# Performance work log

Measured on AMD Instinct MI355X. Metric: run time of the kernel, lower is better.

## Reference

```python
import jax, jax.numpy as jnp
import numpy as np

E = 8        # n_experts
TOP_K = 2    # n_activated_experts
B, T, C = 4, 2048, 2048   # batch, seq, d_model
F = 5632     # expert FFN hidden (SwiGLU)


def setup_inputs() -> dict:
    key = jax.random.key(0)
    k = jax.random.split(key, 5)
    s = 0.02  # init scale keeps activations sane
    return {
        "x":  jax.random.normal(k[0], (B, T, C), jnp.float32),
        "Wg": jax.random.normal(k[1], (C, E), jnp.float32) * s,   # gate Linear (no bias)
        "W1": jax.random.normal(k[2], (E, C, F), jnp.float32) * s, # expert gate proj
        "W3": jax.random.normal(k[3], (E, C, F), jnp.float32) * s, # expert up proj
        "W2": jax.random.normal(k[4], (E, F, C), jnp.float32) * s, # expert down proj
    }


def _moe(x, Wg, W1, W3, W2, top_k=TOP_K, norm_probs=True):
    Bb, Tt, Cc = x.shape
    xf = x.reshape(-1, Cc)                                   # [N, C]
    logits = xf @ Wg                                         # [N, E]
    probs = jax.nn.softmax(logits.astype(jnp.float32), axis=-1)
    probs, indices = jax.lax.top_k(probs, top_k)             # [N, K]
    if norm_probs:
        probs = probs / probs.sum(axis=-1, keepdims=True)
    probs = probs.astype(x.dtype)
    N, Ee = xf.shape[0], W1.shape[0]
    # per-token combine weights: w[n, e] = prob if expert e selected for token n else 0
    # (top_k indices are distinct per token, so at most one add per (n, e))
    w = jnp.zeros((N, Ee), x.dtype).at[jnp.arange(N)[:, None], indices].add(probs)
    # scan over experts: weight-0 tokens contribute nothing, matching the sparse
    # masked dispatch/scatter-add of the original exactly.
    def body(y, ws):
        w1, w3, w2, we = ws                                   # we: [N]
        h = jax.nn.silu(xf @ w1) * (xf @ w3)                  # [N, F]
        return y + we[:, None] * (h @ w2), None
    y, _ = jax.lax.scan(body, jnp.zeros_like(xf), (W1, W3, W2, w.T))
    return y.reshape(Bb, Tt, Cc)


def reference(x, Wg, W1, W3, W2):
    return _moe(x, Wg, W1, W3, W2)
```

## Files before the change

kernel.cpp:

```cpp
#include <hip/hip_runtime.h>

#define N_TOK 8192
#define C_DIM 2048
#define F_DIM 5632
#define E_NUM 8

#define BM 128
#define BN 128
#define BK 64
#define MAXT 136
#define GRID1 (MAXT * (F_DIM/BN))
#define GRID2 (MAXT * (C_DIM/BN))

typedef __attribute__((ext_vector_type(8))) short bf16x8;
typedef __attribute__((ext_vector_type(4))) float f32x4;

typedef const void __attribute__((address_space(1)))* gas1;
typedef void __attribute__((address_space(3)))* las3;

__device__ __forceinline__ unsigned short f2bf(float f){
  union { float f; unsigned u; } v; v.f = f;
  unsigned r = v.u + 0x7FFFu + ((v.u >> 16) & 1u);
  return (unsigned short)(r >> 16);
}

__device__ __forceinline__ void glds16(const unsigned short* g, unsigned short* l){
  __builtin_amdgcn_global_load_lds((gas1)g, (las3)l, 16, 0, 0);
}

__global__ void k_cvt_x(const float* __restrict__ x, unsigned short* __restrict__ xb, int n4){
  int i = blockIdx.x * blockDim.x + threadIdx.x;
  int stride = gridDim.x * blockDim.x;
  const float4* xi = (const float4*)x;
  ushort4* xo = (ushort4*)xb;
  for (; i < n4; i += stride){
    float4 v = xi[i];
    ushort4 o; o.x = f2bf(v.x); o.y = f2bf(v.y); o.z = f2bf(v.z); o.w = f2bf(v.w);
    xo[i] = o;
  }
}

__global__ void k_tcvt_w(const float* __restrict__ in, unsigned short* __restrict__ out, int R, int Cc){
  __shared__ float t[64][65];
  size_t slab = (size_t)blockIdx.z * R * Cc;
  in += slab; out += slab;
  int c0 = blockIdx.x * 64, r0 = blockIdx.y * 64;
  int tx = threadIdx.x, ty = threadIdx.y;
  #pragma unroll
  for (int i = 0; i < 16; ++i){
    int r = ty + i*4;
    t[r][tx] = in[(size_t)(r0 + r) * Cc + c0 + tx];
  }
  __syncthreads();
  #pragma unroll
  for (int i = 0; i < 16; ++i){
    int cr = ty + i*4;
    out[(size_t)(c0 + cr) * R + r0 + tx] = f2bf(t[tx][cr]);
  }
}

__global__ void k_router(const float* __restrict__ x, const float* __restrict__ Wg,
                         int* __restrict__ cnt, int* __restrict__ list, float* __restrict__ p_slot)
{
  int wid = threadIdx.x >> 6, lane = threadIdx.x & 63;
  int n = blockIdx.x * 4 + wid;
  int e = lane >> 3, sub = lane & 7;
  const float* xr = x + (size_t)n * C_DIM;
  float acc = 0.f;
  for (int i = sub; i < C_DIM; i += 8)
    acc += xr[i] * Wg[i*E_NUM + e];
  acc += __shfl_xor(acc, 1);
  acc += __shfl_xor(acc, 2);
  acc += __shfl_xor(acc, 4);
  float lg[E_NUM];
  #pragma unroll
  for (int j = 0; j < E_NUM; ++j) lg[j] = __shfl(acc, j*8);
  if (lane == 0){
    int e1 = 0; float m1 = lg[0];
    #pragma unroll
    for (int j = 1; j < E_NUM; ++j) if (lg[j] > m1){ m1 = lg[j]; e1 = j; }
    int e2 = -1; float m2 = -1e30f;
    #pragma unroll
    for (int j = 0; j < E_NUM; ++j) if (j != e1 && lg[j] > m2){ m2 = lg[j]; e2 = j; }
    float p1 = 1.f / (1.f + __expf(m2 - m1));
    float p2 = 1.f - p1;
    int pos1 = atomicAdd(&cnt[e1], 1);
    list[e1*N_TOK + pos1] = n*2;
    p_slot[n*2] = p1;
    int pos2 = atomicAdd(&cnt[e2], 1);
    list[e2*N_TOK + pos2] = n*2 + 1;
    p_slot[n*2 + 1] = p2;
  }
}

__global__ void k_prefix(const int* __restrict__ cnt, int* __restrict__ meta){
  if (threadIdx.x == 0 && blockIdx.x == 0){
    int acc = 0, t = 0;
    for (int e = 0; e < E_NUM; ++e){
      meta[e] = acc; acc += cnt[e];
      int nt = (cnt[e] + BM - 1) / BM;
      for (int i = 0; i < nt; ++i) meta[16 + t++] = (e << 16) | i;
    }
    meta[8] = t;
  }
}

__global__ __launch_bounds__(256, 2) void k_gemm1(
    const unsigned short* __restrict__ xb,
    const unsigned short* __restrict__ wb1,
    const unsigned short* __restrict__ wb3,
    unsigned short* __restrict__ h,
    const int* __restrict__ cnt,
    const int* __restrict__ meta,
    const int* __restrict__ list)
{
  int o = blockIdx.x;
  int w = (o & 7) * (GRID1/8) + (o >> 3);
  int t = w % MAXT;
  int n0 = (w / MAXT) * BN;
  if (t >= meta[8]) return;
  int info = meta[16 + t];
  int e  = info >> 16;
  int m0 = (info & 0xffff) * BM;
  int count = cnt[e];
  int hbase = meta[e];

  __shared__ __align__(16) unsigned short sA [BM*BK];
  __shared__ __align__(16) unsigned short sB1[BN*BK];
  __shared__ __align__(16) unsigned short sB3[BN*BK];

  int tid = threadIdx.x;
  int lane = tid & 63, wid = tid >> 6;
  int wm = wid >> 1, wn = wid & 1;

  const unsigned short* aS[4];
  const unsigned short* bS[4];
  int swz = (((tid & 7) ^ ((tid >> 3) & 7))) * 8;
  #pragma unroll
  for (int it = 0; it < 4; ++it){
    int row = it*32 + (tid >> 3);
    int ts  = list[e*N_TOK + m0 + row];
    int tok = (ts >> 1) & (N_TOK - 1);
    aS[it] = xb + (size_t)tok * C_DIM + swz;
    bS[it] = wb1 + ((size_t)e*F_DIM + n0 + row) * C_DIM + swz;
  }
  ptrdiff_t w31 = wb3 - wb1;

  f32x4 zero = {0.f, 0.f, 0.f, 0.f};
  f32x4 acc1[4][4], acc3[4][4];
  #pragma unroll
  for (int mi = 0; mi < 4; ++mi)
    #pragma unroll
    for (int ni = 0; ni < 4; ++ni){ acc1[mi][ni] = zero; acc3[mi][ni] = zero; }

  int ldsbase = wid * 512;

  for (int kt = 0; kt < C_DIM/BK; ++kt){
    int ko = kt * BK;
    #pragma unroll
    for (int it = 0; it < 4; ++it){
      glds16(aS[it] + ko,        &sA [it*2048 + ldsbase]);
      glds16(bS[it] + ko,        &sB1[it*2048 + ldsbase]);
      glds16(bS[it] + w31 + ko,  &sB3[it*2048 + ldsbase]);
    }
    __syncthreads();
    #pragma unroll
    for (int ks = 0; ks < 2; ++ks){
      bf16x8 aF[4], b1F[4], b3F[4];
      int xr = ((ks*4 + (lane >> 4)) ^ (lane & 7)) * 8;
      #pragma unroll
      for (int mi = 0; mi < 4; ++mi){
        int r = wm*64 + mi*16 + (lane & 15);
        aF[mi] = *(const bf16x8*)&sA[r*BK + xr];
      }
      #pragma unroll
      for (int ni = 0; ni < 4; ++ni){
        int fr = wn*64 + ni*16 + (lane & 15);
        b1F[ni] = *(const bf16x8*)&sB1[fr*BK + xr];
        b3F[ni] = *(const bf16x8*)&sB3[fr*BK + xr];
      }
      #pragma unroll
      for (int mi = 0; mi < 4; ++mi)
        #pragma unroll
        for (int ni = 0; ni < 4; ++ni){
          acc1[mi][ni] = __builtin_amdgcn_mfma_f32_16x16x32_bf16(aF[mi], b1F[ni], acc1[mi][ni], 0, 0, 0);
          acc3[mi][ni] = __builtin_amdgcn_mfma_f32_16x16x32_bf16(aF[mi], b3F[ni], acc3[mi][ni], 0, 0, 0);
        }
    }
    __syncthreads();
  }

  #pragma unroll
  for (int mi = 0; mi < 4; ++mi){
    #pragma unroll
    for (int r = 0; r < 4; ++r){
      int rloc = m0 + wm*64 + mi*16 + ((lane >> 4) * 4) + r;
      if (rloc < count){
        unsigned short* hrow = h + (size_t)(hbase + rloc) * F_DIM + n0 + wn*64 + (lane & 15);
        #pragma unroll
        for (int ni = 0; ni < 4; ++ni){
          float v1 = acc1[mi][ni][r];
          float v3 = acc3[mi][ni][r];
          float hv = (v1 / (1.f + __expf(-v1))) * v3;
          hrow[ni*16] = f2bf(hv);
        }
      }
    }
  }
}

__global__ __launch_bounds__(256, 2) void k_gemm2(
    const unsigned short* __restrict__ h,
    const unsigned short* __restrict__ wb2,
    float* __restrict__ y,
    const int* __restrict__ cnt,
    const int* __restrict__ meta,
    const int* __restrict__ list,
    const float* __restrict__ p_slot)
{
  int o = blockIdx.x;
  int w = (o & 7) * (GRID2/8) + (o >> 3);
  int t = w % MAXT;
  int n0 = (w / MAXT) * BN;
  if (t >= meta[8]) return;
  int info = meta[16 + t];
  int e  = info >> 16;
  int m0 = (info & 0xffff) * BM;
  int count = cnt[e];
  int hbase = meta[e];

  __shared__ __align__(16) unsigned short sA[BM*BK];
  __shared__ __align__(16) unsigned short sB[BN*BK];

  int tid = threadIdx.x;
  int lane = tid & 63, wid = tid >> 6;
  int wm = wid >> 1, wn = wid & 1;

  const unsigned short* aS[4];
  const unsigned short* bS[4];
  int swz = (((tid & 7) ^ ((tid >> 3) & 7))) * 8;
  #pragma unroll
  for (int it = 0; it < 4; ++it){
    int row = it*32 + (tid >> 3);
    aS[it] = h   + (size_t)(hbase + m0 + row) * F_DIM + swz;
    bS[it] = wb2 + ((size_t)e*C_DIM + n0 + row) * F_DIM + swz;
  }

  f32x4 zero = {0.f, 0.f, 0.f, 0.f};
  f32x4 acc[4][4];
  #pragma unroll
  for (int mi = 0; mi < 4; ++mi)
    #pragma unroll
    for (int ni = 0; ni < 4; ++ni) acc[mi][ni] = zero;

  int ldsbase = wid * 512;

  for (int kt = 0; kt < F_DIM/BK; ++kt){
    int ko = kt * BK;
    #pragma unroll
    for (int it = 0; it < 4; ++it){
      glds16(aS[it] + ko, &sA[it*2048 + ldsbase]);
      glds16(bS[it] + ko, &sB[it*2048 + ldsbase]);
    }
    __syncthreads();
    #pragma unroll
    for (int ks = 0; ks < 2; ++ks){
      bf16x8 aF[4], bF[4];
      int xr = ((ks*4 + (lane >> 4)) ^ (lane & 7)) * 8;
      #pragma unroll
      for (int mi = 0; mi < 4; ++mi){
        int r = wm*64 + mi*16 + (lane & 15);
        aF[mi] = *(const bf16x8*)&sA[r*BK + xr];
      }
      #pragma unroll
      for (int ni = 0; ni < 4; ++ni){
        int cr = wn*64 + ni*16 + (lane & 15);
        bF[ni] = *(const bf16x8*)&sB[cr*BK + xr];
      }
      #pragma unroll
      for (int mi = 0; mi < 4; ++mi)
        #pragma unroll
        for (int ni = 0; ni < 4; ++ni)
          acc[mi][ni] = __builtin_amdgcn_mfma_f32_16x16x32_bf16(aF[mi], bF[ni], acc[mi][ni], 0, 0, 0);
    }
    __syncthreads();
  }

  #pragma unroll
  for (int mi = 0; mi < 4; ++mi){
    #pragma unroll
    for (int r = 0; r < 4; ++r){
      int rloc = m0 + wm*64 + mi*16 + ((lane >> 4) * 4) + r;
      if (rloc < count){
        int ts = list[e*N_TOK + rloc];
        float p = p_slot[ts];
        int tok = ts >> 1;
        float* yr = y + (size_t)tok * C_DIM + n0 + wn*64 + (lane & 15);
        #pragma unroll
        for (int ni = 0; ni < 4; ++ni)
          atomicAdd(&yr[ni*16], p * acc[mi][ni][r]);
      }
    }
  }
}

extern "C" void kernel_launch(void* const* d_in, const int* in_sizes, int n_in,
                              void* d_out, int out_size, void* d_ws, size_t ws_size,
                              hipStream_t stream)
{
  const float* x  = (const float*)d_in[0];
  const float* Wg = (const float*)d_in[1];
  const float* W1 = (const float*)d_in[2];
  const float* W3 = (const float*)d_in[3];
  const float* W2 = (const float*)d_in[4];
  float* y = (float*)d_out;
  (void)in_sizes; (void)n_in; (void)out_size; (void)ws_size;

  char* ws = (char*)d_ws;
  size_t o = 0;
  auto alloc = [&](size_t bytes)->char* {
    char* p = ws + o;
    o = (o + bytes + 255) & ~(size_t)255;
    return p;
  };
  int*    cnt    = (int*)  alloc(E_NUM * 4);
  int*    meta   = (int*)  alloc(160 * 4);
  float*  p_slot = (float*)alloc((size_t)2*N_TOK * 4);
  int*    list   = (int*)  alloc((size_t)E_NUM*N_TOK * 4);
  unsigned short* xb  = (unsigned short*)alloc((size_t)N_TOK*C_DIM * 2);
  unsigned short* wb1 = (unsigned short*)alloc((size_t)E_NUM*C_DIM*F_DIM * 2);
  unsigned short* wb3 = (unsigned short*)alloc((size_t)E_NUM*C_DIM*F_DIM * 2);
  unsigned short* wb2 = (unsigned short*)alloc((size_t)E_NUM*C_DIM*F_DIM * 2);
  unsigned short* h   = (unsigned short*)alloc((size_t)(2*N_TOK + 1024)*F_DIM * 2);

  hipMemsetAsync(cnt, 0, E_NUM * 4, stream);
  hipMemsetAsync(y, 0, (size_t)N_TOK * C_DIM * 4, stream);
  k_cvt_x<<<4096, 256, 0, stream>>>(x, xb, (N_TOK*C_DIM)/4);
  k_tcvt_w<<<dim3(F_DIM/64, C_DIM/64, E_NUM), dim3(64,4), 0, stream>>>(W1, wb1, C_DIM, F_DIM);
  k_tcvt_w<<<dim3(F_DIM/64, C_DIM/64, E_NUM), dim3(64,4), 0, stream>>>(W3, wb3, C_DIM, F_DIM);
  k_tcvt_w<<<dim3(C_DIM/64, F_DIM/64, E_NUM), dim3(64,4), 0, stream>>>(W2, wb2, F_DIM, C_DIM);
  k_router<<<N_TOK/4, 256, 0, stream>>>(x, Wg, cnt, list, p_slot);
  k_prefix<<<1, 64, 0, stream>>>(cnt, meta);
  k_gemm1<<<GRID1, 256, 0, stream>>>(xb, wb1, wb3, h, cnt, meta, list);
  k_gemm2<<<GRID2, 256, 0, stream>>>(h, wb2, y, cnt, meta, list, p_slot);
}
```

Measured before the change: 1.996 ms.

## Double-buffer expert GEMMs with 256-row tiles, 512 threads and phased MFMA scheduling

Both expert GEMM kernels are rebuilt around 256-row token tiles and 512-thread blocks. They use a double-buffered LDS ring loaded by global_load_lds, so the tiles for k+1 and k+2 are prefetched while the current tile is computed. The MFMA work is split into barrier-separated phases with s_setprio and explicit vmcnt waits, and the down-projection GEMM widens to 256 output columns. The goal is to hide global-load latency and raise data reuse per block, at the cost of more LDS per block, heavier register pressure and prefetch reads past the end of the K loop. The router also switches to float4 loads of x.

```diff
diff --git a/kernel.cpp b/kernel.cpp
--- a/kernel.cpp
+++ b/kernel.cpp
@@ -4,13 +4,16 @@
 #define C_DIM 2048
 #define F_DIM 5632
 #define E_NUM 8
-
-#define BM 128
-#define BN 128
 #define BK 64
-#define MAXT 136
-#define GRID1 (MAXT * (F_DIM/BN))
-#define GRID2 (MAXT * (C_DIM/BN))
+
+#define BM 256
+#define MAXT 72
+#define BN1 128
+#define GRID1 (MAXT * (F_DIM/BN1))
+#define BN2 256
+#define GRID2 (MAXT * (C_DIM/BN2))
+#define NT1 (C_DIM/BK)
+#define NT2 (F_DIM/BK)
 
 typedef __attribute__((ext_vector_type(8))) short bf16x8;
 typedef __attribute__((ext_vector_type(4))) float f32x4;
@@ -27,6 +30,8 @@
 __device__ __forceinline__ void glds16(const unsigned short* g, unsigned short* l){
   __builtin_amdgcn_global_load_lds((gas1)g, (las3)l, 16, 0, 0);
 }
+
+#define MFMA_BF16 __builtin_amdgcn_mfma_f32_16x16x32_bf16
 
 __global__ void k_cvt_x(const float* __restrict__ x, unsigned short* __restrict__ xb, int n4){
   int i = blockIdx.x * blockDim.x + threadIdx.x;
@@ -67,8 +72,13 @@
   int e = lane >> 3, sub = lane & 7;
   const float* xr = x + (size_t)n * C_DIM;
   float acc = 0.f;
-  for (int i = sub; i < C_DIM; i += 8)
-    acc += xr[i] * Wg[i*E_NUM + e];
+  for (int i0 = sub*4; i0 < C_DIM; i0 += 32){
+    float4 v = *(const float4*)&xr[i0];
+    acc += v.x * Wg[(i0  )*E_NUM + e];
+    acc += v.y * Wg[(i0+1)*E_NUM + e];
+    acc += v.z * Wg[(i0+2)*E_NUM + e];
+    acc += v.w * Wg[(i0+3)*E_NUM + e];
+  }
   acc += __shfl_xor(acc, 1);
   acc += __shfl_xor(acc, 2);
   acc += __shfl_xor(acc, 4);
@@ -105,7 +115,12 @@
   }
 }
 
-__global__ __launch_bounds__(256, 2) void k_gemm1(
+#define PHASE_ENTER() do{ __builtin_amdgcn_sched_barrier(0); __builtin_amdgcn_s_barrier(); \
+                          __builtin_amdgcn_s_setprio(1); } while(0)
+#define PHASE_EXIT()  do{ __builtin_amdgcn_s_setprio(0); __builtin_amdgcn_sched_barrier(0); \
+                          __builtin_amdgcn_s_barrier(); } while(0)
+
+__global__ __launch_bounds__(512, 2) void k_gemm1(
     const unsigned short* __restrict__ xb,
     const unsigned short* __restrict__ wb1,
     const unsigned short* __restrict__ wb3,
@@ -117,7 +132,7 @@
   int o = blockIdx.x;
   int w = (o & 7) * (GRID1/8) + (o >> 3);
   int t = w % MAXT;
-  int n0 = (w / MAXT) * BN;
+  int n0 = (w / MAXT) * BN1;
   if (t >= meta[8]) return;
   int info = meta[16 + t];
   int e  = info >> 16;
@@ -125,91 +140,122 @@
   int count = cnt[e];
   int hbase = meta[e];
 
-  __shared__ __align__(16) unsigned short sA [BM*BK];
-  __shared__ __align__(16) unsigned short sB1[BN*BK];
-  __shared__ __align__(16) unsigned short sB3[BN*BK];
+  __shared__ __align__(16) unsigned short lds[2*32768];
 
   int tid = threadIdx.x;
   int lane = tid & 63, wid = tid >> 6;
   int wm = wid >> 1, wn = wid & 1;
-
-  const unsigned short* aS[4];
-  const unsigned short* bS[4];
-  int swz = (((tid & 7) ^ ((tid >> 3) & 7))) * 8;
-  #pragma unroll
-  for (int it = 0; it < 4; ++it){
-    int row = it*32 + (tid >> 3);
-    int ts  = list[e*N_TOK + m0 + row];
+  int l15 = lane & 15;
+  int xc0 = (lane >> 4) ^ (lane & 7);
+  int xc1 = xc0 ^ 4;
+
+  int srow = tid >> 3;
+  int swz = ((tid & 7) ^ (srow & 7)) * 8;
+  const unsigned short* aP[4];
+  #pragma unroll
+  for (int u = 0; u < 4; ++u){
+    int ts = list[e*N_TOK + m0 + u*64 + srow];
     int tok = (ts >> 1) & (N_TOK - 1);
-    aS[it] = xb + (size_t)tok * C_DIM + swz;
-    bS[it] = wb1 + ((size_t)e*F_DIM + n0 + row) * C_DIM + swz;
-  }
-  ptrdiff_t w31 = wb3 - wb1;
+    aP[u] = xb + (size_t)tok * C_DIM + swz;
+  }
+  const unsigned short* bP[4];
+  #pragma unroll
+  for (int u = 0; u < 4; ++u){
+    const unsigned short* base = (u < 2) ? wb1 : wb3;
+    bP[u] = base + ((size_t)e*F_DIM + n0 + (u & 1)*64 + srow) * C_DIM + swz;
+  }
+  int ldw = wid * 512;
+
+  #define ST_A(u, kt) glds16(aP[u] + (kt)*BK, &lds[((kt)&1)*32768 + (u)*4096 + ldw])
+  #define ST_B(u, kt) glds16(bP[u] + (kt)*BK, &lds[((kt)&1)*32768 + 16384 + (u)*4096 + ldw])
+
+  ST_A(0,0); ST_A(1,0); ST_A(2,0); ST_A(3,0);
+  ST_B(0,0); ST_B(1,0); ST_B(2,0); ST_B(3,0);
+  ST_A(0,1); ST_A(1,1); ST_A(2,1); ST_A(3,1);
+  asm volatile("s_waitcnt vmcnt(4)" ::: "memory");
+  __builtin_amdgcn_sched_barrier(0);
+  __builtin_amdgcn_s_barrier();
 
   f32x4 zero = {0.f, 0.f, 0.f, 0.f};
   f32x4 acc1[4][4], acc3[4][4];
   #pragma unroll
-  for (int mi = 0; mi < 4; ++mi)
-    #pragma unroll
-    for (int ni = 0; ni < 4; ++ni){ acc1[mi][ni] = zero; acc3[mi][ni] = zero; }
-
-  int ldsbase = wid * 512;
-
-  for (int kt = 0; kt < C_DIM/BK; ++kt){
-    int ko = kt * BK;
-    #pragma unroll
-    for (int it = 0; it < 4; ++it){
-      glds16(aS[it] + ko,        &sA [it*2048 + ldsbase]);
-      glds16(bS[it] + ko,        &sB1[it*2048 + ldsbase]);
-      glds16(bS[it] + w31 + ko,  &sB3[it*2048 + ldsbase]);
-    }
-    __syncthreads();
-    #pragma unroll
-    for (int ks = 0; ks < 2; ++ks){
-      bf16x8 aF[4], b1F[4], b3F[4];
-      int xr = ((ks*4 + (lane >> 4)) ^ (lane & 7)) * 8;
+  for (int m = 0; m < 4; ++m)
+    #pragma unroll
+    for (int q = 0; q < 4; ++q){ acc1[m][q] = zero; acc3[m][q] = zero; }
+
+  for (int kt = 0; kt < NT1; ++kt){
+    const unsigned short* bufc = &lds[(kt & 1)*32768];
+    bf16x8 a[4][2], b1f[2], b3f[2];
+    #pragma unroll
+    for (int m = 0; m < 4; ++m){
+      int row = wm*64 + m*16 + l15;
+      a[m][0] = *(const bf16x8*)&bufc[row*64 + xc0*8];
+      a[m][1] = *(const bf16x8*)&bufc[row*64 + xc1*8];
+    }
+    {
+      int brow = wn*64 + l15;
+      b1f[0] = *(const bf16x8*)&bufc[16384 + brow*64 + xc0*8];
+      b1f[1] = *(const bf16x8*)&bufc[16384 + brow*64 + xc1*8];
+      b3f[0] = *(const bf16x8*)&bufc[24576 + brow*64 + xc0*8];
+      b3f[1] = *(const bf16x8*)&bufc[24576 + brow*64 + xc1*8];
+    }
+    ST_B(0, kt+1); ST_B(1, kt+1); ST_B(2, kt+1); ST_B(3, kt+1);
+    PHASE_ENTER();
+    #pragma unroll
+    for (int m = 0; m < 4; ++m){
+      acc1[m][0] = MFMA_BF16(a[m][0], b1f[0], acc1[m][0], 0, 0, 0);
+      acc1[m][0] = MFMA_BF16(a[m][1], b1f[1], acc1[m][0], 0, 0, 0);
+      acc3[m][0] = MFMA_BF16(a[m][0], b3f[0], acc3[m][0], 0, 0, 0);
+      acc3[m][0] = MFMA_BF16(a[m][1], b3f[1], acc3[m][0], 0, 0, 0);
+    }
+    PHASE_EXIT();
+    #pragma unroll
+    for (int q = 1; q < 4; ++q){
+      int brow = wn*64 + q*16 + l15;
+      b1f[0] = *(const bf16x8*)&bufc[16384 + brow*64 + xc0*8];
+      b1f[1] = *(const bf16x8*)&bufc[16384 + brow*64 + xc1*8];
+      b3f[0] = *(const bf16x8*)&bufc[24576 + brow*64 + xc0*8];
+      b3f[1] = *(const bf16x8*)&bufc[24576 + brow*64 + xc1*8];
+      if (q == 1){ ST_A(0, kt+2); ST_A(1, kt+2); }
+      if (q == 2){ ST_A(2, kt+2); ST_A(3, kt+2); }
+      PHASE_ENTER();
       #pragma unroll
-      for (int mi = 0; mi < 4; ++mi){
-        int r = wm*64 + mi*16 + (lane & 15);
-        aF[mi] = *(const bf16x8*)&sA[r*BK + xr];
+      for (int m = 0; m < 4; ++m){
+        acc1[m][q] = MFMA_BF16(a[m][0], b1f[0], acc1[m][q], 0, 0, 0);
+        acc1[m][q] = MFMA_BF16(a[m][1], b1f[1], acc1[m][q], 0, 0, 0);
+        acc3[m][q] = MFMA_BF16(a[m][0], b3f[0], acc3[m][q], 0, 0, 0);
+        acc3[m][q] = MFMA_BF16(a[m][1], b3f[1], acc3[m][q], 0, 0, 0);
       }
-      #pragma unroll
-      for (int ni = 0; ni < 4; ++ni){
-        int fr = wn*64 + ni*16 + (lane & 15);
-        b1F[ni] = *(const bf16x8*)&sB1[fr*BK + xr];
-        b3F[ni] = *(const bf16x8*)&sB3[fr*BK + xr];
-      }
-      #pragma unroll
-      for (int mi = 0; mi < 4; ++mi)
+      __builtin_amdgcn_s_setprio(0);
+      if (q == 3) asm volatile("s_waitcnt vmcnt(4)" ::: "memory");
+      __builtin_amdgcn_sched_barrier(0);
+      __builtin_amdgcn_s_barrier();
+    }
+  }
+  asm volatile("s_waitcnt vmcnt(0)" ::: "memory");
+
+  #pragma unroll
+  for (int m = 0; m < 4; ++m){
+    #pragma unroll
+    for (int r = 0; r < 4; ++r){
+      int rloc = m0 + wm*64 + m*16 + ((lane >> 4) * 4) + r;
+      if (rloc < count){
+        unsigned short* hrow = h + (size_t)(hbase + rloc) * F_DIM + n0 + wn*64 + l15;
         #pragma unroll
-        for (int ni = 0; ni < 4; ++ni){
-          acc1[mi][ni] = __builtin_amdgcn_mfma_f32_16x16x32_bf16(aF[mi], b1F[ni], acc1[mi][ni], 0, 0, 0);
-          acc3[mi][ni] = __builtin_amdgcn_mfma_f32_16x16x32_bf16(aF[mi], b3F[ni], acc3[mi][ni], 0, 0, 0);
-        }
-    }
-    __syncthreads();
-  }
-
-  #pragma unroll
-  for (int mi = 0; mi < 4; ++mi){
-    #pragma unroll
-    for (int r = 0; r < 4; ++r){
-      int rloc = m0 + wm*64 + mi*16 + ((lane >> 4) * 4) + r;
-      if (rloc < count){
-        unsigned short* hrow = h + (size_t)(hbase + rloc) * F_DIM + n0 + wn*64 + (lane & 15);
-        #pragma unroll
-        for (int ni = 0; ni < 4; ++ni){
-          float v1 = acc1[mi][ni][r];
-          float v3 = acc3[mi][ni][r];
+        for (int q = 0; q < 4; ++q){
+          float v1 = acc1[m][q][r];
+          float v3 = acc3[m][q][r];
           float hv = (v1 / (1.f + __expf(-v1))) * v3;
-          hrow[ni*16] = f2bf(hv);
+          hrow[q*16] = f2bf(hv);
         }
       }
     }
   }
-}
-
-__global__ __launch_bounds__(256, 2) void k_gemm2(
+  #undef ST_A
+  #undef ST_B
+}
+
+__global__ __launch_bounds__(512, 2) void k_gemm2(
     const unsigned short* __restrict__ h,
     const unsigned short* __restrict__ wb2,
     float* __restrict__ y,
@@ -221,7 +267,7 @@
   int o = blockIdx.x;
   int w = (o & 7) * (GRID2/8) + (o >> 3);
   int t = w % MAXT;
-  int n0 = (w / MAXT) * BN;
+  int n0 = (w / MAXT) * BN2;
   if (t >= meta[8]) return;
   int info = meta[16 + t];
   int e  = info >> 16;
@@ -229,79 +275,116 @@
   int count = cnt[e];
   int hbase = meta[e];
 
-  __shared__ __align__(16) unsigned short sA[BM*BK];
-  __shared__ __align__(16) unsigned short sB[BN*BK];
+  __shared__ __align__(16) unsigned short lds[2*32768];
 
   int tid = threadIdx.x;
   int lane = tid & 63, wid = tid >> 6;
   int wm = wid >> 1, wn = wid & 1;
-
-  const unsigned short* aS[4];
-  const unsigned short* bS[4];
-  int swz = (((tid & 7) ^ ((tid >> 3) & 7))) * 8;
-  #pragma unroll
-  for (int it = 0; it < 4; ++it){
-    int row = it*32 + (tid >> 3);
-    aS[it] = h   + (size_t)(hbase + m0 + row) * F_DIM + swz;
-    bS[it] = wb2 + ((size_t)e*C_DIM + n0 + row) * F_DIM + swz;
-  }
+  int l15 = lane & 15;
+  int xc0 = (lane >> 4) ^ (lane & 7);
+  int xc1 = xc0 ^ 4;
+
+  int srow = tid >> 3;
+  int swz = ((tid & 7) ^ (srow & 7)) * 8;
+  const unsigned short* aP[4];
+  #pragma unroll
+  for (int u = 0; u < 4; ++u)
+    aP[u] = h + (size_t)(hbase + m0 + u*64 + srow) * F_DIM + swz;
+  const unsigned short* bP[4];
+  #pragma unroll
+  for (int u = 0; u < 4; ++u)
+    bP[u] = wb2 + ((size_t)e*C_DIM + n0 + u*64 + srow) * F_DIM + swz;
+  int ldw = wid * 512;
+
+  #define ST_A2(u, kt) glds16(aP[u] + (kt)*BK, &lds[((kt)&1)*32768 + (u)*4096 + ldw])
+  #define ST_B2(u, kt) glds16(bP[u] + (kt)*BK, &lds[((kt)&1)*32768 + 16384 + (u)*4096 + ldw])
+
+  ST_A2(0,0); ST_A2(1,0); ST_A2(2,0); ST_A2(3,0);
+  ST_B2(0,0); ST_B2(1,0); ST_B2(2,0); ST_B2(3,0);
+  asm volatile("s_waitcnt vmcnt(4)" ::: "memory");
+  ST_A2(0,1); ST_A2(1,1); ST_A2(2,1); ST_A2(3,1);
+  ST_B2(0,1); ST_B2(2,1);
+  asm volatile("s_waitcnt vmcnt(6)" ::: "memory");
+  __builtin_amdgcn_sched_barrier(0);
+  __builtin_amdgcn_s_barrier();
 
   f32x4 zero = {0.f, 0.f, 0.f, 0.f};
-  f32x4 acc[4][4];
-  #pragma unroll
-  for (int mi = 0; mi < 4; ++mi)
-    #pragma unroll
-    for (int ni = 0; ni < 4; ++ni) acc[mi][ni] = zero;
-
-  int ldsbase = wid * 512;
-
-  for (int kt = 0; kt < F_DIM/BK; ++kt){
-    int ko = kt * BK;
-    #pragma unroll
-    for (int it = 0; it < 4; ++it){
-      glds16(aS[it] + ko, &sA[it*2048 + ldsbase]);
-      glds16(bS[it] + ko, &sB[it*2048 + ldsbase]);
-    }
-    __syncthreads();
-    #pragma unroll
-    for (int ks = 0; ks < 2; ++ks){
-      bf16x8 aF[4], bF[4];
-      int xr = ((ks*4 + (lane >> 4)) ^ (lane & 7)) * 8;
+  f32x4 acc[4][8];
+  #pragma unroll
+  for (int m = 0; m < 4; ++m)
+    #pragma unroll
+    for (int nf = 0; nf < 8; ++nf) acc[m][nf] = zero;
+
+  for (int kt = 0; kt < NT2; ++kt){
+    const unsigned short* bufc = &lds[(kt & 1)*32768];
+    bf16x8 a[4][2], bf[2][2];
+    #pragma unroll
+    for (int m = 0; m < 4; ++m){
+      int row = wm*64 + m*16 + l15;
+      a[m][0] = *(const bf16x8*)&bufc[row*64 + xc0*8];
+      a[m][1] = *(const bf16x8*)&bufc[row*64 + xc1*8];
+    }
+    #pragma unroll
+    for (int j = 0; j < 2; ++j){
+      int brow = wn*128 + j*16 + l15;
+      bf[j][0] = *(const bf16x8*)&bufc[16384 + brow*64 + xc0*8];
+      bf[j][1] = *(const bf16x8*)&bufc[16384 + brow*64 + xc1*8];
+    }
+    ST_B2(1, kt+1); ST_B2(3, kt+1);
+    PHASE_ENTER();
+    #pragma unroll
+    for (int m = 0; m < 4; ++m)
       #pragma unroll
-      for (int mi = 0; mi < 4; ++mi){
-        int r = wm*64 + mi*16 + (lane & 15);
-        aF[mi] = *(const bf16x8*)&sA[r*BK + xr];
+      for (int j = 0; j < 2; ++j){
+        acc[m][j] = MFMA_BF16(a[m][0], bf[j][0], acc[m][j], 0, 0, 0);
+        acc[m][j] = MFMA_BF16(a[m][1], bf[j][1], acc[m][j], 0, 0, 0);
       }
+    PHASE_EXIT();
+    #pragma unroll
+    for (int q = 1; q < 4; ++q){
       #pragma unroll
-      for (int ni = 0; ni < 4; ++ni){
-        int cr = wn*64 + ni*16 + (lane & 15);
-        bF[ni] = *(const bf16x8*)&sB[cr*BK + xr];
+      for (int j = 0; j < 2; ++j){
+        int brow = wn*128 + (q*2 + j)*16 + l15;
+        bf[j][0] = *(const bf16x8*)&bufc[16384 + brow*64 + xc0*8];
+        bf[j][1] = *(const bf16x8*)&bufc[16384 + brow*64 + xc1*8];
       }
+      if (q == 1){ ST_A2(0, kt+2); ST_A2(1, kt+2); }
+      if (q == 2){ ST_A2(2, kt+2); ST_A2(3, kt+2); }
+      if (q == 3){ ST_B2(0, kt+2); ST_B2(2, kt+2); }
+      PHASE_ENTER();
       #pragma unroll
-      for (int mi = 0; mi < 4; ++mi)
+      for (int m = 0; m < 4; ++m)
         #pragma unroll
-        for (int ni = 0; ni < 4; ++ni)
-          acc[mi][ni] = __builtin_amdgcn_mfma_f32_16x16x32_bf16(aF[mi], bF[ni], acc[mi][ni], 0, 0, 0);
-    }
-    __syncthreads();
-  }
-
-  #pragma unroll
-  for (int mi = 0; mi < 4; ++mi){
+        for (int j = 0; j < 2; ++j){
+          acc[m][q*2+j] = MFMA_BF16(a[m][0], bf[j][0], acc[m][q*2+j], 0, 0, 0);
+          acc[m][q*2+j] = MFMA_BF16(a[m][1], bf[j][1], acc[m][q*2+j], 0, 0, 0);
+        }
+      __builtin_amdgcn_s_setprio(0);
+      if (q == 3) asm volatile("s_waitcnt vmcnt(6)" ::: "memory");
+      __builtin_amdgcn_sched_barrier(0);
+      __builtin_amdgcn_s_barrier();
+    }
+  }
+  asm volatile("s_waitcnt vmcnt(0)" ::: "memory");
+
+  #pragma unroll
+  for (int m = 0; m < 4; ++m){
     #pragma unroll
     for (int r = 0; r < 4; ++r){
-      int rloc = m0 + wm*64 + mi*16 + ((lane >> 4) * 4) + r;
+      int rloc = m0 + wm*64 + m*16 + ((lane >> 4) * 4) + r;
       if (rloc < count){
         int ts = list[e*N_TOK + rloc];
         float p = p_slot[ts];
         int tok = ts >> 1;
-        float* yr = y + (size_t)tok * C_DIM + n0 + wn*64 + (lane & 15);
+        float* yr = y + (size_t)tok * C_DIM + n0 + wn*128 + l15;
         #pragma unroll
-        for (int ni = 0; ni < 4; ++ni)
-          atomicAdd(&yr[ni*16], p * acc[mi][ni][r]);
+        for (int nf = 0; nf < 8; ++nf)
+          atomicAdd(&yr[nf*16], p * acc[m][nf][r]);
       }
     }
   }
+  #undef ST_A2
+  #undef ST_B2
 }
 
 extern "C" void kernel_launch(void* const* d_in, const int* in_sizes, int n_in,
@@ -341,6 +424,6 @@
   k_tcvt_w<<<dim3(C_DIM/64, F_DIM/64, E_NUM), dim3(64,4), 0, stream>>>(W2, wb2, F_DIM, C_DIM);
   k_router<<<N_TOK/4, 256, 0, stream>>>(x, Wg, cnt, list, p_slot);
   k_prefix<<<1, 64, 0, stream>>>(cnt, meta);
-  k_gemm1<<<GRID1, 256, 0, stream>>>(xb, wb1, wb3, h, cnt, meta, list);
-  k_gemm2<<<GRID2, 256, 0, stream>>>(h, wb2, y, cnt, meta, list, p_slot);
-}
+  k_gemm1<<<GRID1, 512, 0, stream>>>(xb, wb1, wb3, h, cnt, meta, list);
+  k_gemm2<<<GRID2, 512, 0, stream>>>(h, wb2, y, cnt, meta, list, p_slot);
+}
```

Measured after the change: 1.829 ms. 1.09x faster.
